# Kernel optimization log

Measured on AMD Instinct MI355X. Metric: run time of the kernel, lower is better.

## Reference

```python
import jax, jax.numpy as jnp
import numpy as np

D_MODEL = 512
D_EMB = 300
D_FIXED = 30000
D_EXT = 32000
BS, L, J, N, T = 8, 256, 48, 32, 48


def setup_inputs() -> dict:
    key = jax.random.key(0)
    ks = jax.random.split(key, 32)
    s = 0.02
    def nrm(k, shape, scale=0.02):
        return jax.random.normal(k, shape, dtype=jnp.float32) * scale
    inp = {
        "Mp": jax.random.normal(ks[0], (BS, L, D_MODEL), dtype=jnp.float32),
        "Mq": jax.random.normal(ks[1], (BS, J, D_MODEL), dtype=jnp.float32),
        "Mqa": jax.random.normal(ks[2], (BS, N, D_MODEL), dtype=jnp.float32),
        "Mnlg": jax.random.normal(ks[3], (BS, T, D_MODEL), dtype=jnp.float32),
        "mask_p": jnp.ones((BS, L, 1), dtype=bool),
        "mask_q": jnp.ones((BS, J, 1), dtype=bool),
        "mask_qa": jnp.ones((BS, N, 1), dtype=bool),
        "source_ext": jax.random.randint(ks[4], (BS, L + J + N), 0, D_EXT, dtype=jnp.int64) if jax.config.jax_enable_x64 else jax.random.randint(ks[4], (BS, L + J + N), 0, D_EXT).astype(jnp.int32),
        "special_mask": jnp.ones((D_FIXED,), dtype=bool).at[jnp.array([0, 1, 2, 3])].set(False),
        "d_ext_vocab": D_EXT,
    }
    # additive attention params for question / qa / passage branches
    names = ["q", "a", "p"]
    for i, nme in enumerate(names):
        base = 5 + 5 * i
        inp[f"Wk_{nme}"] = nrm(ks[base + 0], (D_MODEL, D_MODEL))
        inp[f"bk_{nme}"] = jnp.zeros((D_MODEL,), dtype=jnp.float32)
        inp[f"Wq_{nme}"] = nrm(ks[base + 1], (D_MODEL, D_MODEL))
        inp[f"bq_{nme}"] = jnp.zeros((D_MODEL,), dtype=jnp.float32)
        inp[f"v_{nme}"] = nrm(ks[base + 2], (D_MODEL,))
    # vocab generator: Linear(d_model, d_emb) -> Linear(d_emb, d_fixed, bias=False)
    inp["W1"] = nrm(ks[20], (D_MODEL, D_EMB))
    inp["b1"] = jnp.zeros((D_EMB,), dtype=jnp.float32)
    inp["W2"] = nrm(ks[21], (D_EMB, D_FIXED))
    # mixture: Linear(4*d_model, 4) + softmax
    inp["Wm"] = nrm(ks[22], (4 * D_MODEL, 4))
    inp["bm"] = jnp.zeros((4,), dtype=jnp.float32)
    return inp


def _additive_attn(K, V, Q, mask, Wk, bk, Wq, bq, v):
    # K,V: [b,S,d]; Q: [b,T,d]; mask: [b,S,1] bool
    Kp = K @ Wk + bk                                  # [b,S,d]
    Qp = Q @ Wq + bq                                  # [b,T,d]
    scores = jnp.einsum("btsd,d->bts", jnp.tanh(Qp[:, :, None, :] + Kp[:, None, :, :]), v)
    scores = jnp.where(mask[:, None, :, 0], scores, -1e9)
    attn = jax.nn.softmax(scores, axis=-1)            # [b,T,S]
    ctx = jnp.einsum("bts,bsd->btd", attn, V)         # [b,T,d]
    return ctx, attn


def reference(Mp, Mq, Mqa, Mnlg, mask_p, mask_q, mask_qa, source_ext, special_mask,
              Wk_q, bk_q, Wq_q, bq_q, v_q,
              Wk_a, bk_a, Wq_a, bq_a, v_a,
              Wk_p, bk_p, Wq_p, bq_p, v_p,
              W1, b1, W2, Wm, bm, d_ext_vocab):
    d_fixed = special_mask.shape[0]
    bs, Tq, _ = Mnlg.shape

    ctx_q, q_distr = _additive_attn(Mq, Mq, Mnlg, mask_q, Wk_q, bk_q, Wq_q, bq_q, v_q)
    ctx_a, qa_distr = _additive_attn(Mqa, Mqa, Mnlg, mask_qa, Wk_a, bk_a, Wq_a, bq_a, v_a)
    ctx_p, p_distr = _additive_attn(Mp, Mp, Mnlg, mask_p, Wk_p, bk_p, Wq_p, bq_p, v_p)

    # fixed-vocab distribution with special tokens masked out
    logits = (Mnlg @ W1 + b1) @ W2                    # [b,T,d_fixed]
    logits = jnp.where(special_mask[None, None, :], logits, -1e9)
    fixed_vocab_distr = jax.nn.softmax(logits, axis=-1)

    # mixture weights
    mix_in = jnp.concatenate([Mnlg, ctx_q, ctx_a, ctx_p], axis=-1)  # [b,T,4d]
    lambdas = jax.nn.softmax(mix_in @ Wm + bm, axis=-1)             # [b,T,4]
    lam_v, lam_q, lam_qa, lam_p = jnp.split(lambdas, 4, axis=-1)

    fixed_vocab_distr = fixed_vocab_distr * lam_v
    source_distr = jnp.concatenate([p_distr * lam_p, q_distr * lam_q, qa_distr * lam_qa], axis=-1)  # [b,T,S_tot]

    # scatter-add over extended vocab (math-equivalent to one_hot + matmul)
    def _scatter(src, idx):
        # src: [T,S_tot], idx: [S_tot]
        return jnp.zeros((Tq, d_ext_vocab), src.dtype).at[:, idx].add(src)

    ext_vocab_distr = jax.vmap(_scatter)(source_distr, source_ext)  # [b,T,d_ext]
    ext_vocab_distr = ext_vocab_distr.at[:, :, :d_fixed].add(fixed_vocab_distr)
    return ext_vocab_distr, lambdas
```

## Files before the change

kernel.cpp:

```cpp
#include <hip/hip_runtime.h>
#include <math.h>

#define BS     8
#define LL     256
#define JJ     48
#define NN     32
#define TT     48
#define DM     512
#define DEMB   300
#define DFIX   30000
#define DEXT   32000
#define SRC_TOT (LL + JJ + NN)
#define ROWS   (BS * TT)
#define NCH    10
#define CH     (DFIX / NCH)

typedef float f32x4  __attribute__((ext_vector_type(4)));
typedef short bf16x8 __attribute__((ext_vector_type(8)));

__device__ __forceinline__ short f2bf(float f) {
    union { float f; unsigned u; } v; v.f = f;
    return (short)((v.u + 0x7FFFu + ((v.u >> 16) & 1u)) >> 16);
}
__device__ __forceinline__ float bf2f(short s) {
    union { unsigned u; float f; } v;
    v.u = ((unsigned)(unsigned short)s) << 16;
    return v.f;
}
__device__ __forceinline__ float fast_exp2(float x) {
#if __has_builtin(__builtin_amdgcn_exp2f)
    return __builtin_amdgcn_exp2f(x);
#else
    return exp2f(x);
#endif
}
__device__ __forceinline__ float fast_rcp(float x) {
#if __has_builtin(__builtin_amdgcn_rcpf)
    return __builtin_amdgcn_rcpf(x);
#else
    return 1.f / x;
#endif
}
__device__ __forceinline__ float fast_tanh(float x) {
    x = fminf(fmaxf(x, -15.f), 15.f);
    const float e = fast_exp2(x * 2.885390082f);
    return (e - 1.f) * fast_rcp(e + 1.f);
}

struct PDesc { const float* src; short* dst; int K, N, Kp, ntx, tiles; };
struct PArgs { PDesc d[8]; int nd; };

__global__ __launch_bounds__(256) void prep_kernel(PArgs pa)
{
    __shared__ short T[64][72];
    int tile = blockIdx.x, g = 0;
    while (g + 1 < pa.nd && tile >= pa.d[g].tiles) { tile -= pa.d[g].tiles; ++g; }
    const PDesc d = pa.d[g];
    const int kt = tile / d.ntx, nt = tile % d.ntx;
    const int k0 = kt * 64, n0 = nt * 64;
    const int tid = threadIdx.x;
    {
        const int n = n0 + (tid & 63);
        #pragma unroll
        for (int p = 0; p < 16; ++p) {
            const int kk = p * 4 + (tid >> 6);
            const int k = k0 + kk;
            float v = 0.f;
            if (k < d.K && n < d.N) v = d.src[(size_t)k * d.N + n];
            T[kk][tid & 63] = f2bf(v);
        }
    }
    __syncthreads();
    {
        const int kk = (tid & 31) * 2;
        #pragma unroll
        for (int p = 0; p < 8; ++p) {
            const int nn = p * 8 + (tid >> 5);
            const int n = n0 + nn;
            if (n >= d.N) continue;
            short2 s = { T[kk][nn], T[kk + 1][nn] };
            *(short2*)&d.dst[(size_t)n * d.Kp + k0 + kk] = s;
        }
    }
}

struct GDesc { const float* A; const short* Bt; const float* bias; void* C;
               int M, N, K, Kp, nx, my, obf, tiles; };
struct GArgs { GDesc d[7]; int nd; };

__global__ __launch_bounds__(256) void gemm_bf16_kernel(GArgs ga)
{
    __shared__ short As[2][4][130][8];
    __shared__ short Bs[2][4][130][8];

    int tile = blockIdx.x, g = 0;
    while (g + 1 < ga.nd && tile >= ga.d[g].tiles) { tile -= ga.d[g].tiles; ++g; }
    const float* __restrict__ A  = ga.d[g].A;
    const short* __restrict__ Bt = ga.d[g].Bt;
    const float* bias = ga.d[g].bias;
    const int N = ga.d[g].N, K = ga.d[g].K, Kp = ga.d[g].Kp;
    const int nx = ga.d[g].nx, my = ga.d[g].my, obf = ga.d[g].obf;

    int bm, bn;
    if (my > 0) { bm = (tile % my) * 128; bn = (tile / my) * 128; }
    else        { bm = (tile / nx) * 128; bn = (tile % nx) * 128; }
    const int tid  = threadIdx.x;
    const int lane = tid & 63;
    const int wv   = tid >> 6;
    const int wm   = (wv >> 1) * 64;
    const int wn   = (wv & 1) * 64;

    const int a_kq  = (tid & 7) * 4;
    const int a_row = tid >> 3;
    float4  ra[4];
    bf16x8  rb[2];

    auto loadA = [&](int k0) {
        #pragma unroll
        for (int p = 0; p < 4; ++p) {
            const int row = p * 32 + a_row;
            const int gk = k0 + a_kq;
            const float* ap = A + (size_t)(bm + row) * K + gk;
            float4 a = make_float4(0.f, 0.f, 0.f, 0.f);
            if (gk + 3 < K) a = *(const float4*)ap;
            else {
                if (gk     < K) a.x = ap[0];
                if (gk + 1 < K) a.y = ap[1];
                if (gk + 2 < K) a.z = ap[2];
                if (gk + 3 < K) a.w = ap[3];
            }
            ra[p] = a;
        }
    };
    auto loadB = [&](int k0) {
        #pragma unroll
        for (int p = 0; p < 2; ++p) {
            const int idx = p * 256 + tid;
            const int n = idx >> 2, kb = idx & 3;
            const int gn = bn + n;
            bf16x8 v = {};
            if (gn < N) v = *(const bf16x8*)&Bt[(size_t)gn * Kp + k0 + kb * 8];
            rb[p] = v;
        }
    };
    auto storeA = [&](int buf) {
        const int kb = a_kq >> 3, ko = a_kq & 7;
        #pragma unroll
        for (int p = 0; p < 4; ++p) {
            const int row = p * 32 + a_row;
            short4 s = { f2bf(ra[p].x), f2bf(ra[p].y), f2bf(ra[p].z), f2bf(ra[p].w) };
            *(short4*)&As[buf][kb][row][ko] = s;
        }
    };
    auto storeB = [&](int buf) {
        #pragma unroll
        for (int p = 0; p < 2; ++p) {
            const int idx = p * 256 + tid;
            const int n = idx >> 2, kb = idx & 3;
            *(bf16x8*)&Bs[buf][kb][n][0] = rb[p];
        }
    };

    f32x4 acc[4][4] = {};
    const int nk = Kp / 32;

    loadA(0); loadB(0);
    storeA(0); storeB(0);
    __syncthreads();

    for (int kk = 0; kk < nk; ++kk) {
        const int cur = kk & 1;
        if (kk + 1 < nk) { loadA((kk + 1) * 32); loadB((kk + 1) * 32); }
        bf16x8 af[4], bfr[4];
        #pragma unroll
        for (int i = 0; i < 4; ++i) {
            af[i]  = *(const bf16x8*)&As[cur][lane >> 4][wm + i * 16 + (lane & 15)][0];
            bfr[i] = *(const bf16x8*)&Bs[cur][lane >> 4][wn + i * 16 + (lane & 15)][0];
        }
        #pragma unroll
        for (int mi = 0; mi < 4; ++mi)
            #pragma unroll
            for (int ni = 0; ni < 4; ++ni)
                acc[mi][ni] = __builtin_amdgcn_mfma_f32_16x16x32_bf16(
                    af[mi], bfr[ni], acc[mi][ni], 0, 0, 0);
        if (kk + 1 < nk) { storeA(cur ^ 1); storeB(cur ^ 1); }
        __syncthreads();
    }

    #pragma unroll
    for (int ni = 0; ni < 4; ++ni) {
        const int gn = bn + wn + ni * 16 + (lane & 15);
        if (gn >= N) continue;
        const float bb = bias ? bias[gn] : 0.f;
        if (!obf) {
            float* Cf = (float*)ga.d[g].C;
            #pragma unroll
            for (int mi = 0; mi < 4; ++mi)
                #pragma unroll
                for (int r = 0; r < 4; ++r) {
                    const int gm = bm + wm + mi * 16 + (lane >> 4) * 4 + r;
                    Cf[(size_t)gm * N + gn] = acc[mi][ni][r] + bb;
                }
        } else {
            short* Cs = (short*)ga.d[g].C;
            #pragma unroll
            for (int mi = 0; mi < 4; ++mi)
                #pragma unroll
                for (int r = 0; r < 4; ++r) {
                    const int gm = bm + wm + mi * 16 + (lane >> 4) * 4 + r;
                    Cs[(size_t)gm * N + gn] = f2bf(acc[mi][ni][r] + bb);
                }
        }
    }
}

struct SDesc { const float* Kp; const float* Qp; const float* vv;
               int Sb, s0, cnt, off; };
struct SArgs { SDesc c[6]; };

__global__ __launch_bounds__(256) void scores_kernel(SArgs sa,
                                                     float* __restrict__ scb)
{
    const SDesc d = sa.c[blockIdx.y];
    const int bt   = blockIdx.x;
    const int b    = bt / TT;
    const int tid  = threadIdx.x;
    const int lane = tid & 63;
    const int wave = tid >> 6;

    float qp[8], vv[8];
    {
        const float4* q4 = (const float4*)(d.Qp + (size_t)bt * DM) + lane * 2;
        float4 a = q4[0], c = q4[1];
        qp[0]=a.x; qp[1]=a.y; qp[2]=a.z; qp[3]=a.w;
        qp[4]=c.x; qp[5]=c.y; qp[6]=c.z; qp[7]=c.w;
        const float4* v4 = (const float4*)d.vv + lane * 2;
        a = v4[0]; c = v4[1];
        vv[0]=a.x; vv[1]=a.y; vv[2]=a.z; vv[3]=a.w;
        vv[4]=c.x; vv[5]=c.y; vv[6]=c.z; vv[7]=c.w;
    }
    for (int s = wave; s < d.cnt; s += 4) {
        const float* krow = d.Kp + ((size_t)b * d.Sb + d.s0 + s) * DM + lane * 8;
        const float4 ka = ((const float4*)krow)[0];
        const float4 kb = ((const float4*)krow)[1];
        float acc = 0.f;
        acc = fmaf(vv[0], fast_tanh(qp[0] + ka.x), acc);
        acc = fmaf(vv[1], fast_tanh(qp[1] + ka.y), acc);
        acc = fmaf(vv[2], fast_tanh(qp[2] + ka.z), acc);
        acc = fmaf(vv[3], fast_tanh(qp[3] + ka.w), acc);
        acc = fmaf(vv[4], fast_tanh(qp[4] + kb.x), acc);
        acc = fmaf(vv[5], fast_tanh(qp[5] + kb.y), acc);
        acc = fmaf(vv[6], fast_tanh(qp[6] + kb.z), acc);
        acc = fmaf(vv[7], fast_tanh(qp[7] + kb.w), acc);
        #pragma unroll
        for (int off = 32; off; off >>= 1) acc += __shfl_xor(acc, off);
        if (lane == 0) scb[(size_t)bt * SRC_TOT + d.off + s] = acc;
    }
}

__global__ __launch_bounds__(512) void attn2mix_kernel(
    const float* __restrict__ scb,
    const float* __restrict__ Mq, const float* __restrict__ Mqa,
    const float* __restrict__ Mp, const float* __restrict__ Mnlg,
    const float* __restrict__ Wm, const float* __restrict__ bm,
    float* __restrict__ dQ, float* __restrict__ dQA, float* __restrict__ dP,
    float* __restrict__ lam_ws, float* __restrict__ lam_out)
{
    __shared__ float a_sh[SRC_TOT];
    __shared__ float cQ[DM], cA[DM], cP[DM];
    __shared__ float red[16];
    __shared__ float redm[32];
    const int bt   = blockIdx.x;
    const int b    = bt / TT;
    const int tid  = threadIdx.x;
    const int lane = tid & 63;
    const int wave = tid >> 6;
    const float* srow = scb + (size_t)bt * SRC_TOT;

    #pragma unroll
    for (int br = 0; br < 3; ++br) {
        const int off = (br == 0) ? 0 : (br == 1) ? JJ : (JJ + NN);
        const int cnt = (br == 0) ? JJ : (br == 1) ? NN : LL;
        float x = (tid < cnt) ? srow[off + tid] : -INFINITY;
        float m = x;
        #pragma unroll
        for (int o = 32; o; o >>= 1) m = fmaxf(m, __shfl_xor(m, o));
        if (lane == 0) red[wave] = m;
        __syncthreads();
        m = red[0];
        #pragma unroll
        for (int w = 1; w < 8; ++w) m = fmaxf(m, red[w]);
        float e = (tid < cnt) ? __expf(x - m) : 0.f;
        float ss = e;
        #pragma unroll
        for (int o = 32; o; o >>= 1) ss += __shfl_xor(ss, o);
        if (lane == 0) red[8 + wave] = ss;
        __syncthreads();
        float denom = 0.f;
        #pragma unroll
        for (int w = 0; w < 8; ++w) denom += red[8 + w];
        if (tid < cnt) {
            const float a = e / denom;
            a_sh[off + tid] = a;
            float* dst = (br == 0) ? dQ : (br == 1) ? dQA : dP;
            dst[(size_t)bt * cnt + tid] = a;
        }
        __syncthreads();
    }
    {
        float aQ = 0.f, aA = 0.f, aP = 0.f;
        for (int s = 0; s < JJ; ++s)
            aQ = fmaf(a_sh[s],           Mq [((size_t)b * JJ + s) * DM + tid], aQ);
        for (int s = 0; s < NN; ++s)
            aA = fmaf(a_sh[JJ + s],      Mqa[((size_t)b * NN + s) * DM + tid], aA);
        for (int s = 0; s < LL; ++s)
            aP = fmaf(a_sh[JJ + NN + s], Mp [((size_t)b * LL + s) * DM + tid], aP);
        cQ[tid] = aQ; cA[tid] = aA; cP[tid] = aP;
    }
    __syncthreads();
    {
        const float x0 = Mnlg[(size_t)bt * DM + tid];
        const float x1 = cQ[tid], x2 = cA[tid], x3 = cP[tid];
        const float4 w0 = *(const float4*)&Wm[(size_t)tid * 4];
        const float4 w1 = *(const float4*)&Wm[(size_t)(512 + tid) * 4];
        const float4 w2 = *(const float4*)&Wm[(size_t)(1024 + tid) * 4];
        const float4 w3 = *(const float4*)&Wm[(size_t)(1536 + tid) * 4];
        float acc[4];
        acc[0] = x0 * w0.x + x1 * w1.x + x2 * w2.x + x3 * w3.x;
        acc[1] = x0 * w0.y + x1 * w1.y + x2 * w2.y + x3 * w3.y;
        acc[2] = x0 * w0.z + x1 * w1.z + x2 * w2.z + x3 * w3.z;
        acc[3] = x0 * w0.w + x1 * w1.w + x2 * w2.w + x3 * w3.w;
        #pragma unroll
        for (int c = 0; c < 4; ++c)
            #pragma unroll
            for (int o = 32; o; o >>= 1) acc[c] += __shfl_xor(acc[c], o);
        if (lane == 0) {
            redm[wave * 4 + 0] = acc[0]; redm[wave * 4 + 1] = acc[1];
            redm[wave * 4 + 2] = acc[2]; redm[wave * 4 + 3] = acc[3];
        }
        __syncthreads();
        if (tid == 0) {
            float l[4];
            #pragma unroll
            for (int c = 0; c < 4; ++c) {
                float s = bm[c];
                #pragma unroll
                for (int w = 0; w < 8; ++w) s += redm[w * 4 + c];
                l[c] = s;
            }
            const float mx = fmaxf(fmaxf(l[0], l[1]), fmaxf(l[2], l[3]));
            const float e0 = __expf(l[0] - mx), e1 = __expf(l[1] - mx);
            const float e2 = __expf(l[2] - mx), e3 = __expf(l[3] - mx);
            const float inv = 1.f / (e0 + e1 + e2 + e3);
            lam_ws[bt * 4 + 0] = e0 * inv; lam_out[bt * 4 + 0] = e0 * inv;
            lam_ws[bt * 4 + 1] = e1 * inv; lam_out[bt * 4 + 1] = e1 * inv;
            lam_ws[bt * 4 + 2] = e2 * inv; lam_out[bt * 4 + 2] = e2 * inv;
            lam_ws[bt * 4 + 3] = e3 * inv; lam_out[bt * 4 + 3] = e3 * inv;
        }
    }
}

__device__ __forceinline__ void mask8(const void* smask, bool byteLayout, int i,
                                      int* mb)
{
    if (byteLayout) {
        const uchar4 a = ((const uchar4*)((const unsigned char*)smask + i))[0];
        const uchar4 b = ((const uchar4*)((const unsigned char*)smask + i))[1];
        mb[0]=a.x; mb[1]=a.y; mb[2]=a.z; mb[3]=a.w;
        mb[4]=b.x; mb[5]=b.y; mb[6]=b.z; mb[7]=b.w;
    } else {
        const int* p = (const int*)smask + i;
        #pragma unroll
        for (int j = 0; j < 8; ++j) mb[j] = p[j];
    }
}

__global__ __launch_bounds__(256) void stats_partial_kernel(
    const short* __restrict__ logits, const void* __restrict__ smask,
    float* __restrict__ pstat)
{
    __shared__ float red[4];
    const bool byteLayout = (((const int*)smask)[1] == 0x01010101);
    const int r = blockIdx.x, c = blockIdx.y;
    const int tid = threadIdx.x, lane = tid & 63, wave = tid >> 6;
    const int base = c * CH;
    const short* lrow = logits + (size_t)r * DFIX + base;

    float m = -INFINITY;
    for (int g = tid; g < CH / 8; g += 256) {
        const bf16x8 v = *(const bf16x8*)&lrow[g * 8];
        int mb[8]; mask8(smask, byteLayout, base + g * 8, mb);
        #pragma unroll
        for (int j = 0; j < 8; ++j)
            if (mb[j]) m = fmaxf(m, bf2f(v[j]));
    }
    #pragma unroll
    for (int o = 32; o; o >>= 1) m = fmaxf(m, __shfl_xor(m, o));
    if (lane == 0) red[wave] = m;
    __syncthreads();
    m = fmaxf(fmaxf(red[0], red[1]), fmaxf(red[2], red[3]));
    __syncthreads();

    float s = 0.f;
    for (int g = tid; g < CH / 8; g += 256) {
        const bf16x8 v = *(const bf16x8*)&lrow[g * 8];
        int mb[8]; mask8(smask, byteLayout, base + g * 8, mb);
        #pragma unroll
        for (int j = 0; j < 8; ++j)
            if (mb[j]) s += __expf(bf2f(v[j]) - m);
    }
    #pragma unroll
    for (int o = 32; o; o >>= 1) s += __shfl_xor(s, o);
    if (lane == 0) red[wave] = s;
    __syncthreads();
    if (tid == 0) {
        pstat[(r * NCH + c) * 2 + 0] = m;
        pstat[(r * NCH + c) * 2 + 1] = red[0] + red[1] + red[2] + red[3];
    }
}

__global__ __launch_bounds__(256) void write_kernel(
    const short* __restrict__ logits, const void* __restrict__ smask,
    const float* __restrict__ pstat, const float* __restrict__ lam,
    float* __restrict__ out)
{
    const bool byteLayout = (((const int*)smask)[1] == 0x01010101);
    const int r = blockIdx.x;
    float m = -INFINITY;
    #pragma unroll
    for (int c = 0; c < NCH; ++c) m = fmaxf(m, pstat[(r * NCH + c) * 2]);
    float dsum = 0.f;
    #pragma unroll
    for (int c = 0; c < NCH; ++c) {
        const float pm = pstat[(r * NCH + c) * 2];
        const float ps = pstat[(r * NCH + c) * 2 + 1];
        if (ps > 0.f) dsum += ps * __expf(pm - m);
    }
    const float inv = lam[r * 4 + 0] / dsum;

    const int cbase = blockIdx.y * 4096;
    const short* lrow = logits + (size_t)r * DFIX;
    float* orow = out + (size_t)r * DEXT;
    const int tid = threadIdx.x;
    #pragma unroll
    for (int k = 0; k < 2; ++k) {
        const int i = cbase + k * 2048 + tid * 8;
        if (i >= DEXT) continue;
        float4 o0 = make_float4(0.f, 0.f, 0.f, 0.f);
        float4 o1 = make_float4(0.f, 0.f, 0.f, 0.f);
        if (i < DFIX) {
            const bf16x8 v = *(const bf16x8*)&lrow[i];
            int mb[8]; mask8(smask, byteLayout, i, mb);
            o0.x = mb[0] ? __expf(bf2f(v[0]) - m) * inv : 0.f;
            o0.y = mb[1] ? __expf(bf2f(v[1]) - m) * inv : 0.f;
            o0.z = mb[2] ? __expf(bf2f(v[2]) - m) * inv : 0.f;
            o0.w = mb[3] ? __expf(bf2f(v[3]) - m) * inv : 0.f;
            o1.x = mb[4] ? __expf(bf2f(v[4]) - m) * inv : 0.f;
            o1.y = mb[5] ? __expf(bf2f(v[5]) - m) * inv : 0.f;
            o1.z = mb[6] ? __expf(bf2f(v[6]) - m) * inv : 0.f;
            o1.w = mb[7] ? __expf(bf2f(v[7]) - m) * inv : 0.f;
        }
        *(float4*)&orow[i]     = o0;
        *(float4*)&orow[i + 4] = o1;
    }
}

__global__ __launch_bounds__(512) void scatter_kernel(
    const float* __restrict__ lambdas,
    const float* __restrict__ dP, const float* __restrict__ dQ,
    const float* __restrict__ dQA, const void* __restrict__ src_ext,
    float* __restrict__ out)
{
    const int* s32 = (const int*)src_ext;
    const bool src64 = (s32[1] == 0 && s32[3] == 0 && s32[5] == 0 && s32[7] == 0);
    const int r = blockIdx.x;
    const int b = r / TT;
    const int p = threadIdx.x;
    if (p >= SRC_TOT) return;
    float* orow = out + (size_t)r * DEXT;
    const float lamq  = lambdas[r * 4 + 1];
    const float lamqa = lambdas[r * 4 + 2];
    const float lamp  = lambdas[r * 4 + 3];
    const int pos = b * SRC_TOT + p;
    const int idx = src64 ? (int)((const long long*)src_ext)[pos] : s32[pos];
    float val;
    if      (p < LL)      val = dP [(size_t)r * LL + p]             * lamp;
    else if (p < LL + JJ) val = dQ [(size_t)r * JJ + (p - LL)]      * lamq;
    else                  val = dQA[(size_t)r * NN + (p - LL - JJ)] * lamqa;
    atomicAdd(&orow[idx], val);
}

extern "C" void kernel_launch(void* const* d_in, const int* in_sizes, int n_in,
                              void* d_out, int out_size, void* d_ws, size_t ws_size,
                              hipStream_t stream)
{
    const float* Mp   = (const float*)d_in[0];
    const float* Mq   = (const float*)d_in[1];
    const float* Mqa  = (const float*)d_in[2];
    const float* Mnlg = (const float*)d_in[3];
    const void* src_ext = d_in[7];
    const void* smask   = d_in[8];
    const float* Wk_q = (const float*)d_in[10];
    const float* bk_q = (const float*)d_in[11];
    const float* Wq_q = (const float*)d_in[12];
    const float* bq_q = (const float*)d_in[13];
    const float* v_q  = (const float*)d_in[14];
    const float* Wk_a = (const float*)d_in[15];
    const float* bk_a = (const float*)d_in[16];
    const float* Wq_a = (const float*)d_in[17];
    const float* bq_a = (const float*)d_in[18];
    const float* v_a  = (const float*)d_in[19];
    const float* Wk_p = (const float*)d_in[20];
    const float* bk_p = (const float*)d_in[21];
    const float* Wq_p = (const float*)d_in[22];
    const float* bq_p = (const float*)d_in[23];
    const float* v_p  = (const float*)d_in[24];
    const float* W1   = (const float*)d_in[25];
    const float* b1   = (const float*)d_in[26];
    const float* W2   = (const float*)d_in[27];
    const float* Wm   = (const float*)d_in[28];
    const float* bm   = (const float*)d_in[29];
    float* out = (float*)d_out;

    char* ws = (char*)d_ws;
    size_t off = 0;
    auto alloc = [&](size_t bytes) -> char* {
        char* p = ws + off;
        off += (bytes + 255) & ~(size_t)255;
        return p;
    };
    short* logits = (short*)alloc((size_t)ROWS * DFIX * 2);
    float* KpP    = (float*)alloc((size_t)BS * LL * DM * 4);
    float* KpQ    = (float*)alloc((size_t)BS * JJ * DM * 4);
    float* KpA    = (float*)alloc((size_t)BS * NN * DM * 4);
    float* QpQ    = (float*)alloc((size_t)ROWS * DM * 4);
    float* QpA    = (float*)alloc((size_t)ROWS * DM * 4);
    float* QpP    = (float*)alloc((size_t)ROWS * DM * 4);
    float* Hh     = (float*)alloc((size_t)ROWS * DEMB * 4);
    float* dP     = (float*)alloc((size_t)ROWS * LL * 4);
    float* dQ     = (float*)alloc((size_t)ROWS * JJ * 4);
    float* dQA    = (float*)alloc((size_t)ROWS * NN * 4);
    float* lam    = (float*)alloc((size_t)ROWS * 4 * 4);
    float* pstat  = (float*)alloc((size_t)ROWS * NCH * 2 * 4);
    float* scb    = (float*)alloc((size_t)ROWS * SRC_TOT * 4);
    short* tWkq = (short*)alloc((size_t)DM * DM * 2);
    short* tWqq = (short*)alloc((size_t)DM * DM * 2);
    short* tWka = (short*)alloc((size_t)DM * DM * 2);
    short* tWqa = (short*)alloc((size_t)DM * DM * 2);
    short* tWkp = (short*)alloc((size_t)DM * DM * 2);
    short* tWqp = (short*)alloc((size_t)DM * DM * 2);
    short* tW1  = (short*)alloc((size_t)DEMB * DM * 2);
    short* tW2  = (short*)alloc((size_t)DFIX * 320 * 2);
    (void)ws_size; (void)in_sizes; (void)n_in; (void)out_size;

    PArgs pa;
    pa.nd = 8;
    pa.d[0] = { Wk_p, tWkp, DM,   DM,   DM,  8,  64 };
    pa.d[1] = { Wk_q, tWkq, DM,   DM,   DM,  8,  64 };
    pa.d[2] = { Wk_a, tWka, DM,   DM,   DM,  8,  64 };
    pa.d[3] = { Wq_q, tWqq, DM,   DM,   DM,  8,  64 };
    pa.d[4] = { Wq_a, tWqa, DM,   DM,   DM,  8,  64 };
    pa.d[5] = { Wq_p, tWqp, DM,   DM,   DM,  8,  64 };
    pa.d[6] = { W1,   tW1,  DM,   DEMB, DM,  5,  40 };
    pa.d[7] = { W2,   tW2,  DEMB, DFIX, 320, 469, 2345 };
    prep_kernel<<<64 * 6 + 40 + 2345, 256, 0, stream>>>(pa);

    GArgs gA;
    gA.nd = 1;
    gA.d[0] = { Mnlg, tW1, b1, Hh, ROWS, DEMB, DM, DM, 3, 0, 0, 9 };
    gemm_bf16_kernel<<<9, 256, 0, stream>>>(gA);

    GArgs gB;
    gB.nd = 7;
    gB.d[0] = { Hh,   tW2,  nullptr, logits, ROWS,  DFIX, DEMB, 320, 235, 3, 1, 705 };
    gB.d[1] = { Mp,   tWkp, bk_p,    KpP,    BS*LL, DM,   DM,   DM,  4,   0, 0,  64 };
    gB.d[2] = { Mq,   tWkq, bk_q,    KpQ,    BS*JJ, DM,   DM,   DM,  4,   0, 0,  12 };
    gB.d[3] = { Mqa,  tWka, bk_a,    KpA,    BS*NN, DM,   DM,   DM,  4,   0, 0,   8 };
    gB.d[4] = { Mnlg, tWqq, bq_q,    QpQ,    ROWS,  DM,   DM,   DM,  4,   0, 0,  12 };
    gB.d[5] = { Mnlg, tWqa, bq_a,    QpA,    ROWS,  DM,   DM,   DM,  4,   0, 0,  12 };
    gB.d[6] = { Mnlg, tWqp, bq_p,    QpP,    ROWS,  DM,   DM,   DM,  4,   0, 0,  12 };
    gemm_bf16_kernel<<<825, 256, 0, stream>>>(gB);

    SArgs sa;
    sa.c[0] = { KpQ, QpQ, v_q, JJ,   0, JJ,  0 };
    sa.c[1] = { KpA, QpA, v_a, NN,   0, NN,  JJ };
    sa.c[2] = { KpP, QpP, v_p, LL,   0, 64,  JJ + NN };
    sa.c[3] = { KpP, QpP, v_p, LL,  64, 64,  JJ + NN + 64 };
    sa.c[4] = { KpP, QpP, v_p, LL, 128, 64,  JJ + NN + 128 };
    sa.c[5] = { KpP, QpP, v_p, LL, 192, 64,  JJ + NN + 192 };
    scores_kernel<<<dim3(ROWS, 6), 256, 0, stream>>>(sa, scb);
    attn2mix_kernel<<<ROWS, 512, 0, stream>>>(scb, Mq, Mqa, Mp, Mnlg, Wm, bm,
                                              dQ, dQA, dP, lam,
                                              out + (size_t)ROWS * DEXT);

    stats_partial_kernel<<<dim3(ROWS, NCH), 256, 0, stream>>>(logits, smask, pstat);
    write_kernel<<<dim3(ROWS, 8), 256, 0, stream>>>(logits, smask, pstat, lam, out);
    scatter_kernel<<<ROWS, 512, 0, stream>>>(lam, dP, dQ, dQA, src_ext, out);
}
```

Measured before the change: 159.7 us.

## Fuse softmax stats into logits GEMM epilogue and merge attention and output kernels

The logits GEMM epilogue now computes per-tile masked row max and sum-exp and writes them to a partial-stats buffer, which removes the separate stats pass over the bf16 logits. The scores and attention/mix kernels are merged into one per-row kernel that keeps the scores in shared memory. The write and scatter kernels are merged into a single 1024-thread kernel. The W2 GEMM is moved to the end of the grouped launch. In exchange, the write kernel must reduce 235 partials per row serially per thread, and the scores work gets fewer blocks.

```diff
diff --git a/kernel.cpp b/kernel.cpp
--- a/kernel.cpp
+++ b/kernel.cpp
@@ -12,8 +12,7 @@
 #define DEXT   32000
 #define SRC_TOT (LL + JJ + NN)
 #define ROWS   (BS * TT)
-#define NCH    10
-#define CH     (DFIX / NCH)
+#define NT     235
 
 typedef float f32x4  __attribute__((ext_vector_type(4)));
 typedef short bf16x8 __attribute__((ext_vector_type(8)));
@@ -45,6 +44,25 @@
     x = fminf(fmaxf(x, -15.f), 15.f);
     const float e = fast_exp2(x * 2.885390082f);
     return (e - 1.f) * fast_rcp(e + 1.f);
+}
+__device__ __forceinline__ bool smask_true(const void* smask, bool byteLayout, int i)
+{
+    if (byteLayout) return ((const unsigned char*)smask)[i] != 0;
+    return ((const int*)smask)[i] != 0;
+}
+__device__ __forceinline__ void mask8(const void* smask, bool byteLayout, int i,
+                                      int* mb)
+{
+    if (byteLayout) {
+        const uchar4 a = ((const uchar4*)((const unsigned char*)smask + i))[0];
+        const uchar4 b = ((const uchar4*)((const unsigned char*)smask + i))[1];
+        mb[0]=a.x; mb[1]=a.y; mb[2]=a.z; mb[3]=a.w;
+        mb[4]=b.x; mb[5]=b.y; mb[6]=b.z; mb[7]=b.w;
+    } else {
+        const int* p = (const int*)smask + i;
+        #pragma unroll
+        for (int j = 0; j < 8; ++j) mb[j] = p[j];
+    }
 }
 
 struct PDesc { const float* src; short* dst; int K, N, Kp, ntx, tiles; };
@@ -85,13 +103,16 @@
 }
 
 struct GDesc { const float* A; const short* Bt; const float* bias; void* C;
-               int M, N, K, Kp, nx, my, obf, tiles; };
+               const void* smask; float* pstat;
+               int M, N, K, Kp, nx, my, obf, nt, tiles; };
 struct GArgs { GDesc d[7]; int nd; };
 
 __global__ __launch_bounds__(256) void gemm_bf16_kernel(GArgs ga)
 {
     __shared__ short As[2][4][130][8];
     __shared__ short Bs[2][4][130][8];
+    __shared__ float pm_s[128][2];
+    __shared__ float ps_s[128][2];
 
     int tile = blockIdx.x, g = 0;
     while (g + 1 < ga.nd && tile >= ga.d[g].tiles) { tile -= ga.d[g].tiles; ++g; }
@@ -187,13 +208,13 @@
         __syncthreads();
     }
 
-    #pragma unroll
-    for (int ni = 0; ni < 4; ++ni) {
-        const int gn = bn + wn + ni * 16 + (lane & 15);
-        if (gn >= N) continue;
-        const float bb = bias ? bias[gn] : 0.f;
-        if (!obf) {
-            float* Cf = (float*)ga.d[g].C;
+    if (!obf) {
+        float* Cf = (float*)ga.d[g].C;
+        #pragma unroll
+        for (int ni = 0; ni < 4; ++ni) {
+            const int gn = bn + wn + ni * 16 + (lane & 15);
+            if (gn >= N) continue;
+            const float bb = bias ? bias[gn] : 0.f;
             #pragma unroll
             for (int mi = 0; mi < 4; ++mi)
                 #pragma unroll
@@ -201,48 +222,110 @@
                     const int gm = bm + wm + mi * 16 + (lane >> 4) * 4 + r;
                     Cf[(size_t)gm * N + gn] = acc[mi][ni][r] + bb;
                 }
-        } else {
-            short* Cs = (short*)ga.d[g].C;
+        }
+    } else {
+        short* Cs = (short*)ga.d[g].C;
+        const void* sm = ga.d[g].smask;
+        const bool byteLayout = (((const int*)sm)[1] == 0x01010101);
+        int mk[4];
+        #pragma unroll
+        for (int ni = 0; ni < 4; ++ni) {
+            const int gn = bn + wn + ni * 16 + (lane & 15);
+            const bool inb = (gn < N);
+            mk[ni] = inb && smask_true(sm, byteLayout, inb ? gn : 0);
+            if (inb) {
+                #pragma unroll
+                for (int mi = 0; mi < 4; ++mi)
+                    #pragma unroll
+                    for (int r = 0; r < 4; ++r) {
+                        const int gm = bm + wm + mi * 16 + (lane >> 4) * 4 + r;
+                        Cs[(size_t)gm * N + gn] = f2bf(acc[mi][ni][r]);
+                    }
+            }
+        }
+        #pragma unroll
+        for (int mi = 0; mi < 4; ++mi) {
             #pragma unroll
-            for (int mi = 0; mi < 4; ++mi)
+            for (int r = 0; r < 4; ++r) {
+                const int rl = wm + mi * 16 + (lane >> 4) * 4 + r;
+                float vmax = -INFINITY;
                 #pragma unroll
-                for (int r = 0; r < 4; ++r) {
-                    const int gm = bm + wm + mi * 16 + (lane >> 4) * 4 + r;
-                    Cs[(size_t)gm * N + gn] = f2bf(acc[mi][ni][r] + bb);
+                for (int ni = 0; ni < 4; ++ni)
+                    if (mk[ni]) vmax = fmaxf(vmax, acc[mi][ni][r]);
+                #pragma unroll
+                for (int o = 1; o < 16; o <<= 1)
+                    vmax = fmaxf(vmax, __shfl_xor(vmax, o));
+                float se = 0.f;
+                #pragma unroll
+                for (int ni = 0; ni < 4; ++ni)
+                    if (mk[ni]) se += __expf(acc[mi][ni][r] - vmax);
+                #pragma unroll
+                for (int o = 1; o < 16; o <<= 1)
+                    se += __shfl_xor(se, o);
+                if ((lane & 15) == 0) {
+                    pm_s[rl][wn >> 6] = vmax;
+                    ps_s[rl][wn >> 6] = se;
                 }
-        }
-    }
-}
-
-struct SDesc { const float* Kp; const float* Qp; const float* vv;
-               int Sb, s0, cnt, off; };
-struct SArgs { SDesc c[6]; };
-
-__global__ __launch_bounds__(256) void scores_kernel(SArgs sa,
-                                                     float* __restrict__ scb)
+            }
+        }
+        __syncthreads();
+        if (tid < 128) {
+            const float mA = pm_s[tid][0], mB = pm_s[tid][1];
+            const float sA = ps_s[tid][0], sB = ps_s[tid][1];
+            const float m = fmaxf(mA, mB);
+            float s = 0.f;
+            if (sA > 0.f) s += sA * __expf(mA - m);
+            if (sB > 0.f) s += sB * __expf(mB - m);
+            float* ps = ga.d[g].pstat;
+            const size_t idx = ((size_t)(bm + tid) * ga.d[g].nt + (bn >> 7)) * 2;
+            ps[idx + 0] = m;
+            ps[idx + 1] = s;
+        }
+    }
+}
+
+__global__ __launch_bounds__(512) void scoremix_kernel(
+    const float* __restrict__ KpQ, const float* __restrict__ KpA,
+    const float* __restrict__ KpP,
+    const float* __restrict__ QpQ, const float* __restrict__ QpA,
+    const float* __restrict__ QpP,
+    const float* __restrict__ v_q, const float* __restrict__ v_a,
+    const float* __restrict__ v_p,
+    const float* __restrict__ Mq, const float* __restrict__ Mqa,
+    const float* __restrict__ Mp, const float* __restrict__ Mnlg,
+    const float* __restrict__ Wm, const float* __restrict__ bm,
+    float* __restrict__ dQ, float* __restrict__ dQA, float* __restrict__ dP,
+    float* __restrict__ lam_ws, float* __restrict__ lam_out)
 {
-    const SDesc d = sa.c[blockIdx.y];
+    __shared__ float sc[SRC_TOT];
+    __shared__ float a_sh[SRC_TOT];
+    __shared__ float cQ[DM], cA[DM], cP[DM];
+    __shared__ float red[16];
+    __shared__ float redm[32];
     const int bt   = blockIdx.x;
     const int b    = bt / TT;
     const int tid  = threadIdx.x;
     const int lane = tid & 63;
     const int wave = tid >> 6;
 
-    float qp[8], vv[8];
+    float qpQ[8], qpA[8], qpP[8], vvQ[8], vvA[8], vvP[8];
     {
-        const float4* q4 = (const float4*)(d.Qp + (size_t)bt * DM) + lane * 2;
-        float4 a = q4[0], c = q4[1];
-        qp[0]=a.x; qp[1]=a.y; qp[2]=a.z; qp[3]=a.w;
-        qp[4]=c.x; qp[5]=c.y; qp[6]=c.z; qp[7]=c.w;
-        const float4* v4 = (const float4*)d.vv + lane * 2;
-        a = v4[0]; c = v4[1];
-        vv[0]=a.x; vv[1]=a.y; vv[2]=a.z; vv[3]=a.w;
-        vv[4]=c.x; vv[5]=c.y; vv[6]=c.z; vv[7]=c.w;
-    }
-    for (int s = wave; s < d.cnt; s += 4) {
-        const float* krow = d.Kp + ((size_t)b * d.Sb + d.s0 + s) * DM + lane * 8;
-        const float4 ka = ((const float4*)krow)[0];
-        const float4 kb = ((const float4*)krow)[1];
+        auto ld8 = [&](float (&dst)[8], const float* p) {
+            const float4 a = ((const float4*)p)[0];
+            const float4 c = ((const float4*)p)[1];
+            dst[0]=a.x; dst[1]=a.y; dst[2]=a.z; dst[3]=a.w;
+            dst[4]=c.x; dst[5]=c.y; dst[6]=c.z; dst[7]=c.w;
+        };
+        ld8(qpQ, QpQ + (size_t)bt * DM + lane * 8);
+        ld8(qpA, QpA + (size_t)bt * DM + lane * 8);
+        ld8(qpP, QpP + (size_t)bt * DM + lane * 8);
+        ld8(vvQ, v_q + lane * 8);
+        ld8(vvA, v_a + lane * 8);
+        ld8(vvP, v_p + lane * 8);
+    }
+    auto dot = [&](const float* krow, const float (&qp)[8], const float (&vv)[8]) {
+        const float4 ka = ((const float4*)(krow + lane * 8))[0];
+        const float4 kb = ((const float4*)(krow + lane * 8))[1];
         float acc = 0.f;
         acc = fmaf(vv[0], fast_tanh(qp[0] + ka.x), acc);
         acc = fmaf(vv[1], fast_tanh(qp[1] + ka.y), acc);
@@ -252,36 +335,27 @@
         acc = fmaf(vv[5], fast_tanh(qp[5] + kb.y), acc);
         acc = fmaf(vv[6], fast_tanh(qp[6] + kb.z), acc);
         acc = fmaf(vv[7], fast_tanh(qp[7] + kb.w), acc);
-        #pragma unroll
-        for (int off = 32; off; off >>= 1) acc += __shfl_xor(acc, off);
-        if (lane == 0) scb[(size_t)bt * SRC_TOT + d.off + s] = acc;
-    }
-}
-
-__global__ __launch_bounds__(512) void attn2mix_kernel(
-    const float* __restrict__ scb,
-    const float* __restrict__ Mq, const float* __restrict__ Mqa,
-    const float* __restrict__ Mp, const float* __restrict__ Mnlg,
-    const float* __restrict__ Wm, const float* __restrict__ bm,
-    float* __restrict__ dQ, float* __restrict__ dQA, float* __restrict__ dP,
-    float* __restrict__ lam_ws, float* __restrict__ lam_out)
-{
-    __shared__ float a_sh[SRC_TOT];
-    __shared__ float cQ[DM], cA[DM], cP[DM];
-    __shared__ float red[16];
-    __shared__ float redm[32];
-    const int bt   = blockIdx.x;
-    const int b    = bt / TT;
-    const int tid  = threadIdx.x;
-    const int lane = tid & 63;
-    const int wave = tid >> 6;
-    const float* srow = scb + (size_t)bt * SRC_TOT;
+        return acc;
+    };
+    for (int s = wave; s < SRC_TOT; s += 8) {
+        float acc;
+        if (s < JJ)
+            acc = dot(KpQ + ((size_t)b * JJ + s) * DM, qpQ, vvQ);
+        else if (s < JJ + NN)
+            acc = dot(KpA + ((size_t)b * NN + (s - JJ)) * DM, qpA, vvA);
+        else
+            acc = dot(KpP + ((size_t)b * LL + (s - JJ - NN)) * DM, qpP, vvP);
+        #pragma unroll
+        for (int o = 32; o; o >>= 1) acc += __shfl_xor(acc, o);
+        if (lane == 0) sc[s] = acc;
+    }
+    __syncthreads();
 
     #pragma unroll
     for (int br = 0; br < 3; ++br) {
         const int off = (br == 0) ? 0 : (br == 1) ? JJ : (JJ + NN);
         const int cnt = (br == 0) ? JJ : (br == 1) ? NN : LL;
-        float x = (tid < cnt) ? srow[off + tid] : -INFINITY;
+        float x = (tid < cnt) ? sc[off + tid] : -INFINITY;
         float m = x;
         #pragma unroll
         for (int o = 32; o; o >>= 1) m = fmaxf(m, __shfl_xor(m, o));
@@ -360,91 +434,31 @@
     }
 }
 
-__device__ __forceinline__ void mask8(const void* smask, bool byteLayout, int i,
-                                      int* mb)
-{
-    if (byteLayout) {
-        const uchar4 a = ((const uchar4*)((const unsigned char*)smask + i))[0];
-        const uchar4 b = ((const uchar4*)((const unsigned char*)smask + i))[1];
-        mb[0]=a.x; mb[1]=a.y; mb[2]=a.z; mb[3]=a.w;
-        mb[4]=b.x; mb[5]=b.y; mb[6]=b.z; mb[7]=b.w;
-    } else {
-        const int* p = (const int*)smask + i;
-        #pragma unroll
-        for (int j = 0; j < 8; ++j) mb[j] = p[j];
-    }
-}
-
-__global__ __launch_bounds__(256) void stats_partial_kernel(
-    const short* __restrict__ logits, const void* __restrict__ smask,
-    float* __restrict__ pstat)
-{
-    __shared__ float red[4];
-    const bool byteLayout = (((const int*)smask)[1] == 0x01010101);
-    const int r = blockIdx.x, c = blockIdx.y;
-    const int tid = threadIdx.x, lane = tid & 63, wave = tid >> 6;
-    const int base = c * CH;
-    const short* lrow = logits + (size_t)r * DFIX + base;
-
-    float m = -INFINITY;
-    for (int g = tid; g < CH / 8; g += 256) {
-        const bf16x8 v = *(const bf16x8*)&lrow[g * 8];
-        int mb[8]; mask8(smask, byteLayout, base + g * 8, mb);
-        #pragma unroll
-        for (int j = 0; j < 8; ++j)
-            if (mb[j]) m = fmaxf(m, bf2f(v[j]));
-    }
-    #pragma unroll
-    for (int o = 32; o; o >>= 1) m = fmaxf(m, __shfl_xor(m, o));
-    if (lane == 0) red[wave] = m;
-    __syncthreads();
-    m = fmaxf(fmaxf(red[0], red[1]), fmaxf(red[2], red[3]));
-    __syncthreads();
-
-    float s = 0.f;
-    for (int g = tid; g < CH / 8; g += 256) {
-        const bf16x8 v = *(const bf16x8*)&lrow[g * 8];
-        int mb[8]; mask8(smask, byteLayout, base + g * 8, mb);
-        #pragma unroll
-        for (int j = 0; j < 8; ++j)
-            if (mb[j]) s += __expf(bf2f(v[j]) - m);
-    }
-    #pragma unroll
-    for (int o = 32; o; o >>= 1) s += __shfl_xor(s, o);
-    if (lane == 0) red[wave] = s;
-    __syncthreads();
-    if (tid == 0) {
-        pstat[(r * NCH + c) * 2 + 0] = m;
-        pstat[(r * NCH + c) * 2 + 1] = red[0] + red[1] + red[2] + red[3];
-    }
-}
-
-__global__ __launch_bounds__(256) void write_kernel(
+__global__ __launch_bounds__(1024) void writescatter_kernel(
     const short* __restrict__ logits, const void* __restrict__ smask,
     const float* __restrict__ pstat, const float* __restrict__ lam,
+    const float* __restrict__ dP, const float* __restrict__ dQ,
+    const float* __restrict__ dQA, const void* __restrict__ src_ext,
     float* __restrict__ out)
 {
     const bool byteLayout = (((const int*)smask)[1] == 0x01010101);
     const int r = blockIdx.x;
     float m = -INFINITY;
-    #pragma unroll
-    for (int c = 0; c < NCH; ++c) m = fmaxf(m, pstat[(r * NCH + c) * 2]);
+    for (int c = 0; c < NT; ++c) m = fmaxf(m, pstat[((size_t)r * NT + c) * 2]);
     float dsum = 0.f;
-    #pragma unroll
-    for (int c = 0; c < NCH; ++c) {
-        const float pm = pstat[(r * NCH + c) * 2];
-        const float ps = pstat[(r * NCH + c) * 2 + 1];
+    for (int c = 0; c < NT; ++c) {
+        const float pm = pstat[((size_t)r * NT + c) * 2];
+        const float ps = pstat[((size_t)r * NT + c) * 2 + 1];
         if (ps > 0.f) dsum += ps * __expf(pm - m);
     }
     const float inv = lam[r * 4 + 0] / dsum;
 
-    const int cbase = blockIdx.y * 4096;
     const short* lrow = logits + (size_t)r * DFIX;
     float* orow = out + (size_t)r * DEXT;
     const int tid = threadIdx.x;
     #pragma unroll
-    for (int k = 0; k < 2; ++k) {
-        const int i = cbase + k * 2048 + tid * 8;
+    for (int k = 0; k < 4; ++k) {
+        const int i = (k * 1024 + tid) * 8;
         if (i >= DEXT) continue;
         float4 o0 = make_float4(0.f, 0.f, 0.f, 0.f);
         float4 o1 = make_float4(0.f, 0.f, 0.f, 0.f);
@@ -463,31 +477,22 @@
         *(float4*)&orow[i]     = o0;
         *(float4*)&orow[i + 4] = o1;
     }
-}
-
-__global__ __launch_bounds__(512) void scatter_kernel(
-    const float* __restrict__ lambdas,
-    const float* __restrict__ dP, const float* __restrict__ dQ,
-    const float* __restrict__ dQA, const void* __restrict__ src_ext,
-    float* __restrict__ out)
-{
-    const int* s32 = (const int*)src_ext;
-    const bool src64 = (s32[1] == 0 && s32[3] == 0 && s32[5] == 0 && s32[7] == 0);
-    const int r = blockIdx.x;
-    const int b = r / TT;
-    const int p = threadIdx.x;
-    if (p >= SRC_TOT) return;
-    float* orow = out + (size_t)r * DEXT;
-    const float lamq  = lambdas[r * 4 + 1];
-    const float lamqa = lambdas[r * 4 + 2];
-    const float lamp  = lambdas[r * 4 + 3];
-    const int pos = b * SRC_TOT + p;
-    const int idx = src64 ? (int)((const long long*)src_ext)[pos] : s32[pos];
-    float val;
-    if      (p < LL)      val = dP [(size_t)r * LL + p]             * lamp;
-    else if (p < LL + JJ) val = dQ [(size_t)r * JJ + (p - LL)]      * lamq;
-    else                  val = dQA[(size_t)r * NN + (p - LL - JJ)] * lamqa;
-    atomicAdd(&orow[idx], val);
+    __syncthreads();
+    if (tid < SRC_TOT) {
+        const int* s32 = (const int*)src_ext;
+        const bool src64 = (s32[1] == 0 && s32[3] == 0 && s32[5] == 0 && s32[7] == 0);
+        const int b = r / TT;
+        const float lamq  = lam[r * 4 + 1];
+        const float lamqa = lam[r * 4 + 2];
+        const float lamp  = lam[r * 4 + 3];
+        const int pos = b * SRC_TOT + tid;
+        const int idx = src64 ? (int)((const long long*)src_ext)[pos] : s32[pos];
+        float val;
+        if      (tid < LL)      val = dP [(size_t)r * LL + tid]             * lamp;
+        else if (tid < LL + JJ) val = dQ [(size_t)r * JJ + (tid - LL)]      * lamq;
+        else                    val = dQA[(size_t)r * NN + (tid - LL - JJ)] * lamqa;
+        atomicAdd(&orow[idx], val);
+    }
 }
 
 extern "C" void kernel_launch(void* const* d_in, const int* in_sizes, int n_in,
@@ -541,8 +546,7 @@
     float* dQ     = (float*)alloc((size_t)ROWS * JJ * 4);
     float* dQA    = (float*)alloc((size_t)ROWS * NN * 4);
     float* lam    = (float*)alloc((size_t)ROWS * 4 * 4);
-    float* pstat  = (float*)alloc((size_t)ROWS * NCH * 2 * 4);
-    float* scb    = (float*)alloc((size_t)ROWS * SRC_TOT * 4);
+    float* pstat  = (float*)alloc((size_t)ROWS * NT * 2 * 4);
     short* tWkq = (short*)alloc((size_t)DM * DM * 2);
     short* tWqq = (short*)alloc((size_t)DM * DM * 2);
     short* tWka = (short*)alloc((size_t)DM * DM * 2);
@@ -567,33 +571,33 @@
 
     GArgs gA;
     gA.nd = 1;
-    gA.d[0] = { Mnlg, tW1, b1, Hh, ROWS, DEMB, DM, DM, 3, 0, 0, 9 };
+    gA.d[0] = { Mnlg, tW1, b1, Hh, nullptr, nullptr,
+                ROWS, DEMB, DM, DM, 3, 0, 0, 0, 9 };
     gemm_bf16_kernel<<<9, 256, 0, stream>>>(gA);
 
     GArgs gB;
     gB.nd = 7;
-    gB.d[0] = { Hh,   tW2,  nullptr, logits, ROWS,  DFIX, DEMB, 320, 235, 3, 1, 705 };
-    gB.d[1] = { Mp,   tWkp, bk_p,    KpP,    BS*LL, DM,   DM,   DM,  4,   0, 0,  64 };
-    gB.d[2] = { Mq,   tWkq, bk_q,    KpQ,    BS*JJ, DM,   DM,   DM,  4,   0, 0,  12 };
-    gB.d[3] = { Mqa,  tWka, bk_a,    KpA,    BS*NN, DM,   DM,   DM,  4,   0, 0,   8 };
-    gB.d[4] = { Mnlg, tWqq, bq_q,    QpQ,    ROWS,  DM,   DM,   DM,  4,   0, 0,  12 };
-    gB.d[5] = { Mnlg, tWqa, bq_a,    QpA,    ROWS,  DM,   DM,   DM,  4,   0, 0,  12 };
-    gB.d[6] = { Mnlg, tWqp, bq_p,    QpP,    ROWS,  DM,   DM,   DM,  4,   0, 0,  12 };
+    gB.d[0] = { Mp,   tWkp, bk_p,    KpP,    nullptr, nullptr,
+                BS*LL, DM,   DM,   DM,  4,   0, 0, 0,  64 };
+    gB.d[1] = { Mq,   tWkq, bk_q,    KpQ,    nullptr, nullptr,
+                BS*JJ, DM,   DM,   DM,  4,   0, 0, 0,  12 };
+    gB.d[2] = { Mqa,  tWka, bk_a,    KpA,    nullptr, nullptr,
+                BS*NN, DM,   DM,   DM,  4,   0, 0, 0,   8 };
+    gB.d[3] = { Mnlg, tWqq, bq_q,    QpQ,    nullptr, nullptr,
+                ROWS,  DM,   DM,   DM,  4,   0, 0, 0,  12 };
+    gB.d[4] = { Mnlg, tWqa, bq_a,    QpA,    nullptr, nullptr,
+                ROWS,  DM,   DM,   DM,  4,   0, 0, 0,  12 };
+    gB.d[5] = { Mnlg, tWqp, bq_p,    QpP,    nullptr, nullptr,
+                ROWS,  DM,   DM,   DM,  4,   0, 0, 0,  12 };
+    gB.d[6] = { Hh,   tW2,  nullptr, logits, smask,   pstat,
+                ROWS,  DFIX, DEMB, 320, 235, 3, 1, NT, 705 };
     gemm_bf16_kernel<<<825, 256, 0, stream>>>(gB);
 
-    SArgs sa;
-    sa.c[0] = { KpQ, QpQ, v_q, JJ,   0, JJ,  0 };
-    sa.c[1] = { KpA, QpA, v_a, NN,   0, NN,  JJ };
-    sa.c[2] = { KpP, QpP, v_p, LL,   0, 64,  JJ + NN };
-    sa.c[3] = { KpP, QpP, v_p, LL,  64, 64,  JJ + NN + 64 };
-    sa.c[4] = { KpP, QpP, v_p, LL, 128, 64,  JJ + NN + 128 };
-    sa.c[5] = { KpP, QpP, v_p, LL, 192, 64,  JJ + NN + 192 };
-    scores_kernel<<<dim3(ROWS, 6), 256, 0, stream>>>(sa, scb);
-    attn2mix_kernel<<<ROWS, 512, 0, stream>>>(scb, Mq, Mqa, Mp, Mnlg, Wm, bm,
-                                              dQ, dQA, dP, lam,
-                                              out + (size_t)ROWS * DEXT);
-
-    stats_partial_kernel<<<dim3(ROWS, NCH), 256, 0, stream>>>(logits, smask, pstat);
-    write_kernel<<<dim3(ROWS, 8), 256, 0, stream>>>(logits, smask, pstat, lam, out);
-    scatter_kernel<<<ROWS, 512, 0, stream>>>(lam, dP, dQ, dQA, src_ext, out);
-}
+    scoremix_kernel<<<ROWS, 512, 0, stream>>>(
+        KpQ, KpA, KpP, QpQ, QpA, QpP, v_q, v_a, v_p,
+        Mq, Mqa, Mp, Mnlg, Wm, bm, dQ, dQA, dP,
+        lam, out + (size_t)ROWS * DEXT);
+
+    writescatter_kernel<<<ROWS, 1024, 0, stream>>>(
+        logits, smask, pstat, lam, dP, dQ, dQA, src_ext, out);
+}
```

Result: slower. 255.3 us (+59.9%).
